# Kernel tuning notes

Measured on AMD Instinct MI355X. Metric: run time of the kernel, lower is better.

## Reference

```python
import math
import jax, jax.numpy as jnp
import numpy as np

D_MODEL = 1024
N_POLES = 32        # d_state // 2
DIRECTIONS = 2      # bidirectional
SEQ_LEN = 4096
DT_MIN, DT_MAX = 1e-3, 1e-1


def setup_inputs() -> dict:
    key = jax.random.key(0)
    k_dt, k_c = jax.random.split(key, 2)
    # log_dt ~ U[log(dt_min), log(dt_max)]
    log_dt = jax.random.uniform(k_dt, (D_MODEL,), dtype=jnp.float32) \
        * (math.log(DT_MAX) - math.log(DT_MIN)) + math.log(DT_MIN)
    # S4D-Lin initialization: real part -0.5, imag part pi*n
    log_a_real = jnp.log(0.5 * jnp.ones((D_MODEL, N_POLES), dtype=jnp.float32))
    a_imag = math.pi * jnp.tile(jnp.arange(N_POLES, dtype=jnp.float32)[None, :], (D_MODEL, 1))
    # complex coeffs stored as real view [..., 2]
    coeffs = jax.random.normal(k_c, (DIRECTIONS, D_MODEL, N_POLES, 2), dtype=jnp.float32)
    return {
        "log_dt": log_dt,
        "log_a_real": log_a_real,
        "a_imag": a_imag,
        "coeffs": coeffs,
        "sequence_length": SEQ_LEN,
    }


def reference(log_dt, log_a_real, a_imag, coeffs, sequence_length):
    dt = jnp.exp(log_dt)                                   # [H]
    c = coeffs[..., 0] + 1j * coeffs[..., 1]               # [dir, H, N] complex
    a = -jnp.exp(log_a_real) + 1j * a_imag                 # [H, N] complex
    timeline = jnp.arange(sequence_length, dtype=jnp.float32)  # [L]
    delta_a = a * dt[:, None]                              # [H, N]
    # Vandermonde matrix exp(delta_a * l): [H, N, L] complex (the big intermediate)
    vand = jnp.exp(delta_a[:, :, None] * timeline)
    scaled_c = c * (jnp.exp(delta_a) - 1.0) / a            # [dir, H, N]
    # contract over poles N -> [dir, H, L]
    kernels = 2.0 * jnp.real(jnp.einsum('dhn,hnl->dhl', scaled_c, vand))
    return kernels
```

## Files before the change

kernel.cpp:

```cpp
#include <hip/hip_runtime.h>
#include <math.h>


constexpr int H     = 1024;
constexpr int NP    = 32;
constexpr int L     = 4096;
constexpr int BLOCK = 256;
constexpr int CHUNK = 16;

constexpr float INV2PI = 0.15915494309189535f;
constexpr float TWOPI  = 6.283185307179586f;

__global__ __launch_bounds__(BLOCK)
void ssm_vand_kernel(const float* __restrict__ log_dt,
                     const float* __restrict__ log_a_real,
                     const float* __restrict__ a_imag,
                     const float* __restrict__ coeffs,
                     float* __restrict__ out)
{
    const int h = blockIdx.x;
    const int t = threadIdx.x;

    __shared__ float4 pole[NP * 2];

    if (t < NP) {
        const int n = t;
        const float dt  = expf(log_dt[h]);
        const float ar  = -expf(log_a_real[h * NP + n]);
        const float ai  = a_imag[h * NP + n];
        const float dar = ar * dt;
        const float dai = ai * dt;

        const float e256 = expf(256.0f * dar);
        float rev256 = 256.0f * dai * INV2PI;
        rev256 -= floorf(rev256);
        float s256, c256;
        sincosf(rev256 * TWOPI, &s256, &c256);

        const float ed = expf(dar);
        float sd, cd;
        sincosf(dai, &sd, &cd);
        const float emr = ed * cd - 1.0f;
        const float emi = ed * sd;
        const float inv = 1.0f / (ar * ar + ai * ai);
        const float gr  = (emr * ar + emi * ai) * inv;
        const float gi  = (emi * ar - emr * ai) * inv;

        const float cr0 = coeffs[((0 * H + h) * NP + n) * 2 + 0];
        const float ci0 = coeffs[((0 * H + h) * NP + n) * 2 + 1];
        const float cr1 = coeffs[((1 * H + h) * NP + n) * 2 + 0];
        const float ci1 = coeffs[((1 * H + h) * NP + n) * 2 + 1];

        pole[n * 2 + 0] = make_float4(dar, dai * INV2PI, e256 * c256, e256 * s256);
        pole[n * 2 + 1] = make_float4(cr0 * gr - ci0 * gi,
                                      cr0 * gi + ci0 * gr,
                                      cr1 * gr - ci1 * gi,
                                      cr1 * gi + ci1 * gr);
    }
    __syncthreads();

    float acc0[CHUNK];
    float acc1[CHUNK];
    #pragma unroll
    for (int j = 0; j < CHUNK; ++j) { acc0[j] = 0.0f; acc1[j] = 0.0f; }

    const float lf = (float)t;

    #pragma unroll 1
    for (int n = 0; n < NP; ++n) {
        const float4 p0 = pole[n * 2 + 0];
        const float4 p1 = pole[n * 2 + 1];

        const float e  = __expf(p0.x * lf);
        float rev = p0.y * lf;
        rev -= floorf(rev);
        float s, c;
        __sincosf(rev * TWOPI, &s, &c);
        float wr = e * c;
        float wi = e * s;

        #pragma unroll
        for (int j = 0; j < CHUNK; ++j) {
            acc0[j] = fmaf(p1.x, wr, fmaf(-p1.y, wi, acc0[j]));
            acc1[j] = fmaf(p1.z, wr, fmaf(-p1.w, wi, acc1[j]));
            const float nwr = fmaf(wr, p0.z, -(wi * p0.w));
            wi              = fmaf(wi, p0.z,  (wr * p0.w));
            wr = nwr;
        }
    }

    float* o0 = out + (size_t)h * L + t;
    float* o1 = out + (size_t)(H + h) * L + t;
    #pragma unroll
    for (int j = 0; j < CHUNK; ++j) {
        o0[j * BLOCK] = 2.0f * acc0[j];
        o1[j * BLOCK] = 2.0f * acc1[j];
    }
}

extern "C" void kernel_launch(void* const* d_in, const int* in_sizes, int n_in,
                              void* d_out, int out_size, void* d_ws, size_t ws_size,
                              hipStream_t stream) {
    const float* log_dt     = (const float*)d_in[0];
    const float* log_a_real = (const float*)d_in[1];
    const float* a_imag     = (const float*)d_in[2];
    const float* coeffs     = (const float*)d_in[3];
    float* out = (float*)d_out;

    ssm_vand_kernel<<<dim3(H), dim3(BLOCK), 0, stream>>>(
        log_dt, log_a_real, a_imag, coeffs, out);
}
```

Before: 97.33 us.

## Split each head across two blocks and use double-float phase for accuracy

Each head is now handled by two blocks, each covering half of the sequence, so there are twice as many blocks with CHUNK=8 accumulators per thread instead of 16. Pole setup is duplicated per half. The phase rate is computed in double on setup and split into hi/lo floats so phases at large sequence offsets stay accurate, which adds a few ops per pole in the inner loop. The factor of 2 is folded into the coefficients, and launch bounds now request 8 blocks per CU.

```diff
diff --git a/kernel.cpp b/kernel.cpp
--- a/kernel.cpp
+++ b/kernel.cpp
@@ -2,40 +2,48 @@
 #include <math.h>
 
 
-constexpr int H     = 1024;
-constexpr int NP    = 32;
-constexpr int L     = 4096;
-constexpr int BLOCK = 256;
-constexpr int CHUNK = 16;
+constexpr int H      = 1024;
+constexpr int NP     = 32;
+constexpr int L      = 4096;
+constexpr int BLOCK  = 256;
+constexpr int HALVES = 2;
+constexpr int SEG    = L / HALVES;
+constexpr int CHUNK  = SEG / BLOCK;
 
-constexpr float INV2PI = 0.15915494309189535f;
-constexpr float TWOPI  = 6.283185307179586f;
+constexpr float  TWOPI    = 6.283185307179586f;
+constexpr double INV2PI_D = 0.15915494309189535;
 
-__global__ __launch_bounds__(BLOCK)
+__global__ __launch_bounds__(BLOCK, 8)
 void ssm_vand_kernel(const float* __restrict__ log_dt,
                      const float* __restrict__ log_a_real,
                      const float* __restrict__ a_imag,
                      const float* __restrict__ coeffs,
                      float* __restrict__ out)
 {
-    const int h = blockIdx.x;
-    const int t = threadIdx.x;
+    const int h    = blockIdx.x >> 1;
+    const int half = blockIdx.x & 1;
+    const int t    = threadIdx.x;
 
-    __shared__ float4 pole[NP * 2];
+    __shared__ float4 pole[NP * 3];
 
     if (t < NP) {
         const int n = t;
-        const float dt  = expf(log_dt[h]);
+        const float dtf = expf(log_dt[h]);
         const float ar  = -expf(log_a_real[h * NP + n]);
         const float ai  = a_imag[h * NP + n];
-        const float dar = ar * dt;
-        const float dai = ai * dt;
+        const float dar = ar * dtf;
+        const float dai = ai * dtf;
+
+        const double rate  = (double)ai * (double)dtf * INV2PI_D;
+        const double ratef = rate - floor(rate);
+        const float  rhi   = (float)ratef;
+        const float  rlo   = (float)(ratef - (double)rhi);
 
         const float e256 = expf(256.0f * dar);
-        float rev256 = 256.0f * dai * INV2PI;
-        rev256 -= floorf(rev256);
+        double r256 = 256.0 * rate;
+        r256 -= floor(r256);
         float s256, c256;
-        sincosf(rev256 * TWOPI, &s256, &c256);
+        sincosf((float)r256 * TWOPI, &s256, &c256);
 
         const float ed = expf(dar);
         float sd, cd;
@@ -51,11 +59,12 @@
         const float cr1 = coeffs[((1 * H + h) * NP + n) * 2 + 0];
         const float ci1 = coeffs[((1 * H + h) * NP + n) * 2 + 1];
 
-        pole[n * 2 + 0] = make_float4(dar, dai * INV2PI, e256 * c256, e256 * s256);
-        pole[n * 2 + 1] = make_float4(cr0 * gr - ci0 * gi,
-                                      cr0 * gi + ci0 * gr,
-                                      cr1 * gr - ci1 * gi,
-                                      cr1 * gi + ci1 * gr);
+        pole[n * 3 + 0] = make_float4(dar, rhi, rlo, 0.0f);
+        pole[n * 3 + 1] = make_float4(e256 * c256, e256 * s256, 0.0f, 0.0f);
+        pole[n * 3 + 2] = make_float4(2.0f * (cr0 * gr - ci0 * gi),
+                                      2.0f * (cr0 * gi + ci0 * gr),
+                                      2.0f * (cr1 * gr - ci1 * gi),
+                                      2.0f * (cr1 * gi + ci1 * gr));
     }
     __syncthreads();
 
@@ -64,37 +73,39 @@
     #pragma unroll
     for (int j = 0; j < CHUNK; ++j) { acc0[j] = 0.0f; acc1[j] = 0.0f; }
 
-    const float lf = (float)t;
+    const float lf = (float)(half * SEG + t);
 
     #pragma unroll 1
     for (int n = 0; n < NP; ++n) {
-        const float4 p0 = pole[n * 2 + 0];
-        const float4 p1 = pole[n * 2 + 1];
+        const float4 pa = pole[n * 3 + 0];
+        const float4 pz = pole[n * 3 + 1];
+        const float4 ps = pole[n * 3 + 2];
 
-        const float e  = __expf(p0.x * lf);
-        float rev = p0.y * lf;
-        rev -= floorf(rev);
+        const float m = __expf(pa.x * lf);
+        const float p = pa.y * lf;
+        const float e = fmaf(pa.y, lf, -p);
+        float rev = (p - floorf(p)) + fmaf(pa.z, lf, e);
         float s, c;
         __sincosf(rev * TWOPI, &s, &c);
-        float wr = e * c;
-        float wi = e * s;
+        float wr = m * c;
+        float wi = m * s;
 
         #pragma unroll
         for (int j = 0; j < CHUNK; ++j) {
-            acc0[j] = fmaf(p1.x, wr, fmaf(-p1.y, wi, acc0[j]));
-            acc1[j] = fmaf(p1.z, wr, fmaf(-p1.w, wi, acc1[j]));
-            const float nwr = fmaf(wr, p0.z, -(wi * p0.w));
-            wi              = fmaf(wi, p0.z,  (wr * p0.w));
+            acc0[j] = fmaf(ps.x, wr, fmaf(-ps.y, wi, acc0[j]));
+            acc1[j] = fmaf(ps.z, wr, fmaf(-ps.w, wi, acc1[j]));
+            const float nwr = fmaf(wr, pz.x, -(wi * pz.y));
+            wi              = fmaf(wi, pz.x,  (wr * pz.y));
             wr = nwr;
         }
     }
 
-    float* o0 = out + (size_t)h * L + t;
-    float* o1 = out + (size_t)(H + h) * L + t;
+    float* o0 = out + (size_t)h * L + half * SEG + t;
+    float* o1 = o0 + (size_t)H * L;
     #pragma unroll
     for (int j = 0; j < CHUNK; ++j) {
-        o0[j * BLOCK] = 2.0f * acc0[j];
-        o1[j * BLOCK] = 2.0f * acc1[j];
+        o0[j * BLOCK] = acc0[j];
+        o1[j * BLOCK] = acc1[j];
     }
 }
 
@@ -107,6 +118,6 @@
     const float* coeffs     = (const float*)d_in[3];
     float* out = (float*)d_out;
 
-    ssm_vand_kernel<<<dim3(H), dim3(BLOCK), 0, stream>>>(
+    ssm_vand_kernel<<<dim3(H * HALVES), dim3(BLOCK), 0, stream>>>(
         log_dt, log_a_real, a_imag, coeffs, out);
 }
```

Measured after the change: 98.07 us. No clear change (+0.8%).
